# Kernel tuning notes

Measured on AMD Instinct MI355X. Metric: run time of the kernel, lower is better.

The kernel has to match this reference:

```python
import jax, jax.numpy as jnp
import numpy as np

D_MODEL = 1024
NUM_HEADS = 16
HEAD_DIM = D_MODEL // NUM_HEADS
THETA = 10000.0


def setup_inputs() -> dict:
    key = jax.random.key(0)
    k1, k2, k3 = jax.random.split(key, 3)
    B, S = 4, 2048
    x = jax.random.normal(k1, (B, S, D_MODEL), dtype=jnp.float32)
    token_positions = jnp.arange(S, dtype=jnp.int32)
    std_qkv = 2.0 / (D_MODEL + 3 * D_MODEL)
    std_o = 2.0 / (D_MODEL + D_MODEL)
    W_qkv = jax.random.normal(k2, (3 * D_MODEL, D_MODEL), dtype=jnp.float32) * std_qkv
    W_o = jax.random.normal(k3, (D_MODEL, D_MODEL), dtype=jnp.float32) * std_o
    return {"x": x, "token_positions": token_positions, "W_qkv": W_qkv, "W_o": W_o}


def _apply_rope(x, positions):
    # x: [B, H, S, d]; positions: [S]
    d = x.shape[-1]
    inv_freq = 1.0 / THETA ** (2.0 * jnp.arange(0, d // 2, dtype=jnp.float32) / d)
    angle = positions.astype(jnp.float32)[:, None] * inv_freq[None, :]  # [S, d/2]
    cos, sin = jnp.cos(angle), jnp.sin(angle)
    x1, x2 = x[..., 0::2], x[..., 1::2]
    rot = jnp.stack([x1 * cos - x2 * sin, x2 * cos + x1 * sin], axis=-1)
    return rot.reshape(x.shape)


def reference(x, token_positions, W_qkv, W_o):
    B, S, D = x.shape
    H, hd = NUM_HEADS, HEAD_DIM
    qkv = jnp.einsum('bsi,ji->bsj', x, W_qkv)            # [B, S, 3D]
    qkv = qkv.reshape(B, S, 3, H, hd).transpose(2, 0, 3, 1, 4)  # [3, B, H, S, hd]
    q, k, v = qkv[0], qkv[1], qkv[2]
    q = _apply_rope(q, token_positions)
    k = _apply_rope(k, token_positions)
    scores = jnp.einsum('bhqd,bhkd->bhqk', q, k) / jnp.sqrt(jnp.float32(hd))
    causal = jnp.tril(jnp.ones((S, S), dtype=bool))
    scores = jnp.where(causal, scores, -jnp.inf)
    probs = jax.nn.softmax(scores, axis=-1)
    attn = jnp.einsum('bhqk,bhkd->bhqd', probs, v)       # [B, H, S, hd]
    attn = attn.transpose(0, 2, 1, 3).reshape(B, S, D)
    return jnp.einsum('bsi,ji->bsj', attn, W_o)
```

## Files before the change

### kernel.cpp

```cpp
#include <hip/hip_runtime.h>

#define B_ 4
#define S_ 2048
#define D_ 1024
#define H_ 16
#define HD_ 64
#define M_ (B_*S_)
#define NQKV_ (3*D_)

typedef _Float16 f16;
typedef __attribute__((ext_vector_type(4))) _Float16 f16x4;
typedef __attribute__((ext_vector_type(8))) _Float16 f16x8;
typedef __attribute__((ext_vector_type(4))) float f32x4;

__device__ __forceinline__ void gload_lds16(const void* g, void* lds) {
  __builtin_amdgcn_global_load_lds(
      (const __attribute__((address_space(1))) void*)g,
      (__attribute__((address_space(3))) void*)lds, 16, 0, 0);
}

__global__ void cast_kernel(const float* __restrict__ in, f16* __restrict__ out) {
  size_t i = (size_t)(blockIdx.x * 256 + threadIdx.x) * 8;
  float4 a = *reinterpret_cast<const float4*>(in + i);
  float4 b = *reinterpret_cast<const float4*>(in + i + 4);
  f16x8 o;
  o[0] = (f16)a.x; o[1] = (f16)a.y; o[2] = (f16)a.z; o[3] = (f16)a.w;
  o[4] = (f16)b.x; o[5] = (f16)b.y; o[6] = (f16)b.z; o[7] = (f16)b.w;
  *reinterpret_cast<f16x8*>(out + i) = o;
}

__global__ void rope_kernel(f16* __restrict__ q, f16* __restrict__ k,
                            const int* __restrict__ pos) {
  int idx = blockIdx.x * 256 + threadIdx.x;
  int t = idx & 31;
  int srow = (idx >> 5) & (S_ - 1);
  float p = (float)pos[srow];
  float invf = exp2f((float)t * -0.4152410118609203f);
  float ang = p * invf;
  float sn, cs;
  sincosf(ang, &sn, &cs);
  const float qs = 0.125f * 1.4426950408889634f;
  size_t base = ((size_t)(idx >> 5)) * HD_ + 2 * t;
  float x1 = (float)q[base], x2 = (float)q[base + 1];
  q[base]     = (f16)((x1 * cs - x2 * sn) * qs);
  q[base + 1] = (f16)((x2 * cs + x1 * sn) * qs);
  x1 = (float)k[base]; x2 = (float)k[base + 1];
  k[base]     = (f16)(x1 * cs - x2 * sn);
  k[base + 1] = (f16)(x2 * cs + x1 * sn);
}

__global__ void vtrans_kernel(const f16* __restrict__ v, f16* __restrict__ vt) {
  __shared__ __align__(16) f16 tile[64][72];
  int tid = threadIdx.x;
  int bh = blockIdx.x >> 5;
  int s0 = (blockIdx.x & 31) << 6;
  const size_t vbase = ((size_t)bh * S_ + s0) * HD_;
  #pragma unroll
  for (int i = 0; i < 2; ++i) {
    int f = i * 256 + tid;
    int row = f >> 3, c8 = (f & 7) * 8;
    f16x8 val = *reinterpret_cast<const f16x8*>(v + vbase + (size_t)row * HD_ + c8);
    #pragma unroll
    for (int j = 0; j < 8; ++j) tile[row][c8 + j] = val[j];
  }
  __syncthreads();
  const size_t tbase = (size_t)bh * (HD_ * S_);
  #pragma unroll
  for (int i = 0; i < 2; ++i) {
    int f = i * 256 + tid;
    int d = f >> 3, c8 = (f & 7) * 8;
    f16x8 o;
    #pragma unroll
    for (int j = 0; j < 8; ++j) o[j] = tile[c8 + j][d];
    *reinterpret_cast<f16x8*>(vt + tbase + (size_t)d * S_ + s0 + c8) = o;
  }
}

template <int MODE>
__global__ __launch_bounds__(256)
void gemm_bt(const f16* __restrict__ A, const f16* __restrict__ Bt,
             void* __restrict__ Cout, int M, int N, int K) {
  __shared__ __align__(16) f16 As[128 * 64];
  __shared__ __align__(16) f16 Bs[128 * 64];
  const int tid = threadIdx.x;
  const int w = tid >> 6, l = tid & 63;
  const int nM = M >> 7;
  const int bm = (blockIdx.x % nM) << 7;
  const int bn = (blockIdx.x / nM) << 7;
  const int wr = (w >> 1) << 6;
  const int wc = (w & 1) << 6;
  const int lr = l & 15;
  const int lk = (l >> 4) << 3;
  const int orow = (l >> 4) << 2;
  const int srow = tid >> 3;
  const int sc8 = (tid & 7) * 8;

  f32x4 acc[4][4];
  #pragma unroll
  for (int i = 0; i < 4; ++i)
    #pragma unroll
    for (int j = 0; j < 4; ++j) acc[i][j] = f32x4{0.f, 0.f, 0.f, 0.f};

  for (int k0 = 0; k0 < K; k0 += 64) {
    __syncthreads();
    #pragma unroll
    for (int i = 0; i < 4; ++i) {
      gload_lds16(A + (size_t)(bm + i * 32 + srow) * K + k0 + sc8,
                  (void*)(As + (i * 256 + w * 64) * 8));
      gload_lds16(Bt + (size_t)(bn + i * 32 + srow) * K + k0 + sc8,
                  (void*)(Bs + (i * 256 + w * 64) * 8));
    }
    __syncthreads();
    #pragma unroll
    for (int t = 0; t < 2; ++t) {
      f16x8 af[4], bfr[4];
      #pragma unroll
      for (int mi = 0; mi < 4; ++mi)
        af[mi] = *reinterpret_cast<const f16x8*>(As + (wr + mi * 16 + lr) * 64 + t * 32 + lk);
      #pragma unroll
      for (int ni = 0; ni < 4; ++ni)
        bfr[ni] = *reinterpret_cast<const f16x8*>(Bs + (wc + ni * 16 + lr) * 64 + t * 32 + lk);
      #pragma unroll
      for (int mi = 0; mi < 4; ++mi)
        #pragma unroll
        for (int ni = 0; ni < 4; ++ni)
          acc[mi][ni] = __builtin_amdgcn_mfma_f32_16x16x32_f16(af[mi], bfr[ni], acc[mi][ni], 0, 0, 0);
    }
  }

  if (MODE == 0) {
    f16* qkv = (f16*)Cout;
    const size_t which_stride = (size_t)B_ * H_ * S_ * HD_;
    #pragma unroll
    for (int ni = 0; ni < 4; ++ni) {
      int n = bn + wc + ni * 16 + lr;
      int which = n >> 10, h = (n >> 6) & (H_ - 1), d = n & (HD_ - 1);
      size_t nb = (size_t)which * which_stride + (size_t)h * (S_ * HD_) + d;
      #pragma unroll
      for (int mi = 0; mi < 4; ++mi) {
        #pragma unroll
        for (int r = 0; r < 4; ++r) {
          int m = bm + wr + mi * 16 + orow + r;
          int b = m >> 11, s = m & (S_ - 1);
          qkv[nb + (size_t)b * (H_ * S_ * HD_) + (size_t)s * HD_] = (f16)acc[mi][ni][r];
        }
      }
    }
  } else {
    float* C = (float*)Cout;
    #pragma unroll
    for (int mi = 0; mi < 4; ++mi)
      #pragma unroll
      for (int r = 0; r < 4; ++r) {
        int m = bm + wr + mi * 16 + orow + r;
        #pragma unroll
        for (int ni = 0; ni < 4; ++ni) {
          int n = bn + wc + ni * 16 + lr;
          C[(size_t)m * N + n] = acc[mi][ni][r];
        }
      }
  }
}

__global__ __launch_bounds__(256)
void attn_kernel(const f16* __restrict__ q, const f16* __restrict__ k,
                 const f16* __restrict__ vt, f16* __restrict__ attn_out) {
  __shared__ __align__(16) f16 Ks[64 * 64];
  __shared__ __align__(16) f16 Vs[64 * 64];
  __shared__ __align__(16) f16 Ps[4][16 * 72];
  const int tid = threadIdx.x, w = tid >> 6, l = tid & 63;
  const int lr = l & 15, lk = (l >> 4) << 3, orow = (l >> 4) << 2;
  const int bh = blockIdx.x & 63;
  const int qt = 31 - (int)(blockIdx.x >> 6);
  const int q0 = qt << 6;
  const size_t bhoff = (size_t)bh * (S_ * HD_);
  const size_t vtoff = (size_t)bh * (HD_ * S_);
  const int srow = tid >> 3;
  const int sc8 = (tid & 7) * 8;
  const int ssw = sc8 ^ ((srow & 7) << 3);
  const int swz = (lr & 7) << 3;
  const int h = bh & (H_ - 1), b = bh >> 4;
  const int qg = q0 + w * 16 + lr;

  f16x8 qf[2];
  #pragma unroll
  for (int t = 0; t < 2; ++t)
    qf[t] = *reinterpret_cast<const f16x8*>(q + bhoff + (size_t)qg * HD_ + t * 32 + lk);

  f32x4 o[4];
  float m_run = -1e30f, l_run = 0.f;
  #pragma unroll
  for (int i = 0; i < 4; ++i) o[i] = f32x4{0.f, 0.f, 0.f, 0.f};

  const int ntiles = qt + 1;
  for (int it = 0; it < ntiles; ++it) {
    const int kv0 = it << 6;
    __syncthreads();
    #pragma unroll
    for (int i = 0; i < 2; ++i) {
      gload_lds16(k + bhoff + (size_t)(kv0 + i * 32 + srow) * HD_ + ssw,
                  (void*)(Ks + (i * 256 + w * 64) * 8));
      gload_lds16(vt + vtoff + (size_t)(i * 32 + srow) * S_ + kv0 + ssw,
                  (void*)(Vs + (i * 256 + w * 64) * 8));
    }
    __syncthreads();

    f32x4 sacc[4];
    #pragma unroll
    for (int ni = 0; ni < 4; ++ni) sacc[ni] = f32x4{0.f, 0.f, 0.f, 0.f};
    #pragma unroll
    for (int t = 0; t < 2; ++t) {
      #pragma unroll
      for (int ni = 0; ni < 4; ++ni) {
        f16x8 kf = *reinterpret_cast<const f16x8*>(Ks + (ni * 16 + lr) * 64 + ((t * 32 + lk) ^ swz));
        sacc[ni] = __builtin_amdgcn_mfma_f32_16x16x32_f16(kf, qf[t], sacc[ni], 0, 0, 0);
      }
    }
    if (it == ntiles - 1) {
      #pragma unroll
      for (int ni = 0; ni < 4; ++ni) {
        #pragma unroll
        for (int r = 0; r < 4; ++r) {
          int kvg = kv0 + ni * 16 + orow + r;
          if (kvg > qg) sacc[ni][r] = -1e30f;
        }
      }
    }

    f32x4 m4 = sacc[0];
    #pragma unroll
    for (int ni = 1; ni < 4; ++ni)
      #pragma unroll
      for (int r = 0; r < 4; ++r) m4[r] = fmaxf(m4[r], sacc[ni][r]);
    float mloc = fmaxf(fmaxf(m4[0], m4[1]), fmaxf(m4[2], m4[3]));
    mloc = fmaxf(mloc, __shfl_xor(mloc, 16));
    mloc = fmaxf(mloc, __shfl_xor(mloc, 32));
    float mn = fmaxf(m_run, mloc);
    float scale = exp2f(m_run - mn);
    m_run = mn;
    #pragma unroll
    for (int ni = 0; ni < 4; ++ni)
      #pragma unroll
      for (int r = 0; r < 4; ++r) sacc[ni][r] = exp2f(sacc[ni][r] - mn);
    f32x4 s4 = sacc[0];
    #pragma unroll
    for (int ni = 1; ni < 4; ++ni)
      #pragma unroll
      for (int r = 0; r < 4; ++r) s4[r] += sacc[ni][r];
    float sloc = (s4[0] + s4[1]) + (s4[2] + s4[3]);
    sloc += __shfl_xor(sloc, 16);
    sloc += __shfl_xor(sloc, 32);
    l_run = l_run * scale + sloc;
    #pragma unroll
    for (int ni = 0; ni < 4; ++ni)
      #pragma unroll
      for (int r = 0; r < 4; ++r) o[ni][r] *= scale;

    #pragma unroll
    for (int ni = 0; ni < 4; ++ni) {
      f16x4 pk;
      #pragma unroll
      for (int r = 0; r < 4; ++r) pk[r] = (f16)sacc[ni][r];
      *reinterpret_cast<f16x4*>(&Ps[w][lr * 72 + ni * 16 + orow]) = pk;
    }

    #pragma unroll
    for (int t = 0; t < 2; ++t) {
      f16x8 pf = *reinterpret_cast<const f16x8*>(&Ps[w][lr * 72 + t * 32 + lk]);
      #pragma unroll
      for (int ni = 0; ni < 4; ++ni) {
        f16x8 vf = *reinterpret_cast<const f16x8*>(Vs + (ni * 16 + lr) * 64 + ((t * 32 + lk) ^ swz));
        o[ni] = __builtin_amdgcn_mfma_f32_16x16x32_f16(vf, pf, o[ni], 0, 0, 0);
      }
    }
  }

  float rl = 1.0f / l_run;
  #pragma unroll
  for (int ni = 0; ni < 4; ++ni) {
    f16x4 ov;
    #pragma unroll
    for (int r = 0; r < 4; ++r) ov[r] = (f16)(o[ni][r] * rl);
    *reinterpret_cast<f16x4*>(
        &attn_out[(size_t)(b * S_ + qg) * D_ + h * HD_ + ni * 16 + orow]) = ov;
  }
}

extern "C" void kernel_launch(void* const* d_in, const int* in_sizes, int n_in,
                              void* d_out, int out_size, void* d_ws, size_t ws_size,
                              hipStream_t stream) {
  const float* x    = (const float*)d_in[0];
  const int*   pos  = (const int*)d_in[1];
  const float* wqkv = (const float*)d_in[2];
  const float* wo   = (const float*)d_in[3];
  float* out = (float*)d_out;

  const size_t BHSD = (size_t)B_ * H_ * S_ * HD_;
  f16* xb    = (f16*)d_ws;
  f16* wqkvb = xb + (size_t)M_ * D_;
  f16* wob   = wqkvb + (size_t)NQKV_ * D_;
  f16* qb    = wob + (size_t)D_ * D_;
  f16* kb    = qb + BHSD;
  f16* vb    = kb + BHSD;
  f16* vtb   = vb + BHSD;
  f16* attnb = vtb + BHSD;

  cast_kernel<<<(M_ * D_) / 2048, 256, 0, stream>>>(x, xb);
  cast_kernel<<<(NQKV_ * D_) / 2048, 256, 0, stream>>>(wqkv, wqkvb);
  cast_kernel<<<(D_ * D_) / 2048, 256, 0, stream>>>(wo, wob);

  gemm_bt<0><<<(M_ / 128) * (NQKV_ / 128), 256, 0, stream>>>(xb, wqkvb, (void*)qb, M_, NQKV_, D_);

  rope_kernel<<<(B_ * H_ * S_ * 32) / 256, 256, 0, stream>>>(qb, kb, pos);
  vtrans_kernel<<<B_ * H_ * (S_ / 64), 256, 0, stream>>>(vb, vtb);

  attn_kernel<<<64 * 32, 256, 0, stream>>>(qb, kb, vtb, attnb);

  gemm_bt<1><<<(M_ / 128) * (D_ / 128), 256, 0, stream>>>(attnb, wob, (void*)out, M_, D_, D_);
}
```

Measured before the change: 225.4 us.

## Fuse RoPE and V transpose into QKV GEMM epilogue via precomputed trig table

Swaps the MFMA operand order so each lane holds four consecutive output columns, which allows vectorized epilogue stores. The QKV GEMM epilogue now applies RoPE (with the softmax scale for Q) using a small precomputed cos/sin table and writes V directly in transposed layout. This removes the separate rope and vtrans kernels and their round trips through global memory. The output GEMM also gets float4 stores. The transposed V writes are strided scalar stores, which may be poorly coalesced.

Measured after the change: 216.2 us. 4.1% less time.

```diff
diff --git a/kernel.cpp b/kernel.cpp
--- a/kernel.cpp
+++ b/kernel.cpp
@@ -29,57 +29,22 @@
   *reinterpret_cast<f16x8*>(out + i) = o;
 }
 
-__global__ void rope_kernel(f16* __restrict__ q, f16* __restrict__ k,
-                            const int* __restrict__ pos) {
+__global__ void trig_kernel(const int* __restrict__ pos, float2* __restrict__ tab) {
   int idx = blockIdx.x * 256 + threadIdx.x;
-  int t = idx & 31;
-  int srow = (idx >> 5) & (S_ - 1);
-  float p = (float)pos[srow];
+  int s = idx >> 5, t = idx & 31;
+  float p = (float)pos[s];
   float invf = exp2f((float)t * -0.4152410118609203f);
-  float ang = p * invf;
   float sn, cs;
-  sincosf(ang, &sn, &cs);
-  const float qs = 0.125f * 1.4426950408889634f;
-  size_t base = ((size_t)(idx >> 5)) * HD_ + 2 * t;
-  float x1 = (float)q[base], x2 = (float)q[base + 1];
-  q[base]     = (f16)((x1 * cs - x2 * sn) * qs);
-  q[base + 1] = (f16)((x2 * cs + x1 * sn) * qs);
-  x1 = (float)k[base]; x2 = (float)k[base + 1];
-  k[base]     = (f16)(x1 * cs - x2 * sn);
-  k[base + 1] = (f16)(x2 * cs + x1 * sn);
-}
-
-__global__ void vtrans_kernel(const f16* __restrict__ v, f16* __restrict__ vt) {
-  __shared__ __align__(16) f16 tile[64][72];
-  int tid = threadIdx.x;
-  int bh = blockIdx.x >> 5;
-  int s0 = (blockIdx.x & 31) << 6;
-  const size_t vbase = ((size_t)bh * S_ + s0) * HD_;
-  #pragma unroll
-  for (int i = 0; i < 2; ++i) {
-    int f = i * 256 + tid;
-    int row = f >> 3, c8 = (f & 7) * 8;
-    f16x8 val = *reinterpret_cast<const f16x8*>(v + vbase + (size_t)row * HD_ + c8);
-    #pragma unroll
-    for (int j = 0; j < 8; ++j) tile[row][c8 + j] = val[j];
-  }
-  __syncthreads();
-  const size_t tbase = (size_t)bh * (HD_ * S_);
-  #pragma unroll
-  for (int i = 0; i < 2; ++i) {
-    int f = i * 256 + tid;
-    int d = f >> 3, c8 = (f & 7) * 8;
-    f16x8 o;
-    #pragma unroll
-    for (int j = 0; j < 8; ++j) o[j] = tile[c8 + j][d];
-    *reinterpret_cast<f16x8*>(vt + tbase + (size_t)d * S_ + s0 + c8) = o;
-  }
+  sincosf(p * invf, &sn, &cs);
+  tab[idx] = float2{cs, sn};
 }
 
 template <int MODE>
 __global__ __launch_bounds__(256)
 void gemm_bt(const f16* __restrict__ A, const f16* __restrict__ Bt,
-             void* __restrict__ Cout, int M, int N, int K) {
+             void* __restrict__ Cout, const float2* __restrict__ tab,
+             f16* __restrict__ kout, f16* __restrict__ vtout,
+             int M, int N, int K) {
   __shared__ __align__(16) f16 As[128 * 64];
   __shared__ __align__(16) f16 Bs[128 * 64];
   const int tid = threadIdx.x;
@@ -124,41 +89,61 @@
       for (int mi = 0; mi < 4; ++mi)
         #pragma unroll
         for (int ni = 0; ni < 4; ++ni)
-          acc[mi][ni] = __builtin_amdgcn_mfma_f32_16x16x32_f16(af[mi], bfr[ni], acc[mi][ni], 0, 0, 0);
+          acc[mi][ni] = __builtin_amdgcn_mfma_f32_16x16x32_f16(bfr[ni], af[mi], acc[mi][ni], 0, 0, 0);
     }
   }
 
   if (MODE == 0) {
-    f16* qkv = (f16*)Cout;
-    const size_t which_stride = (size_t)B_ * H_ * S_ * HD_;
-    #pragma unroll
-    for (int ni = 0; ni < 4; ++ni) {
-      int n = bn + wc + ni * 16 + lr;
-      int which = n >> 10, h = (n >> 6) & (H_ - 1), d = n & (HD_ - 1);
-      size_t nb = (size_t)which * which_stride + (size_t)h * (S_ * HD_) + d;
+    const int which = bn >> 10;
+    const int h = ((bn + wc) >> 6) & (H_ - 1);
+    if (which < 2) {
+      f16* dst = which ? kout : (f16*)Cout;
+      const float qs = which ? 1.0f : 0.125f * 1.4426950408889634f;
       #pragma unroll
       for (int mi = 0; mi < 4; ++mi) {
+        int m = bm + wr + mi * 16 + lr;
+        int b = m >> 11, s = m & (S_ - 1);
+        size_t rowbase = ((size_t)(b * H_ + h) * S_ + s) * HD_;
+        const float4* trow = reinterpret_cast<const float4*>(tab + (size_t)s * 32);
         #pragma unroll
-        for (int r = 0; r < 4; ++r) {
-          int m = bm + wr + mi * 16 + orow + r;
-          int b = m >> 11, s = m & (S_ - 1);
-          qkv[nb + (size_t)b * (H_ * S_ * HD_) + (size_t)s * HD_] = (f16)acc[mi][ni][r];
+        for (int ni = 0; ni < 4; ++ni) {
+          int d0 = ni * 16 + orow;
+          float4 cssn = trow[d0 >> 2];
+          float x0 = acc[mi][ni][0], x1 = acc[mi][ni][1];
+          float x2 = acc[mi][ni][2], x3 = acc[mi][ni][3];
+          f16x4 ov;
+          ov[0] = (f16)((x0 * cssn.x - x1 * cssn.y) * qs);
+          ov[1] = (f16)((x1 * cssn.x + x0 * cssn.y) * qs);
+          ov[2] = (f16)((x2 * cssn.z - x3 * cssn.w) * qs);
+          ov[3] = (f16)((x3 * cssn.z + x2 * cssn.w) * qs);
+          *reinterpret_cast<f16x4*>(&dst[rowbase + d0]) = ov;
         }
+      }
+    } else {
+      #pragma unroll
+      for (int mi = 0; mi < 4; ++mi) {
+        int m = bm + wr + mi * 16 + lr;
+        int b = m >> 11, s = m & (S_ - 1);
+        size_t base = (size_t)(b * H_ + h) * (HD_ * S_) + s;
+        #pragma unroll
+        for (int ni = 0; ni < 4; ++ni)
+          #pragma unroll
+          for (int r = 0; r < 4; ++r)
+            vtout[base + (size_t)(ni * 16 + orow + r) * S_] = (f16)acc[mi][ni][r];
       }
     }
   } else {
     float* C = (float*)Cout;
     #pragma unroll
-    for (int mi = 0; mi < 4; ++mi)
-      #pragma unroll
-      for (int r = 0; r < 4; ++r) {
-        int m = bm + wr + mi * 16 + orow + r;
-        #pragma unroll
-        for (int ni = 0; ni < 4; ++ni) {
-          int n = bn + wc + ni * 16 + lr;
-          C[(size_t)m * N + n] = acc[mi][ni][r];
-        }
-      }
+    for (int mi = 0; mi < 4; ++mi) {
+      int m = bm + wr + mi * 16 + lr;
+      #pragma unroll
+      for (int ni = 0; ni < 4; ++ni) {
+        int n = bn + wc + ni * 16 + orow;
+        *reinterpret_cast<float4*>(&C[(size_t)m * N + n]) =
+            float4{acc[mi][ni][0], acc[mi][ni][1], acc[mi][ni][2], acc[mi][ni][3]};
+      }
+    }
   }
 }
 
@@ -301,20 +286,20 @@
   f16* wob   = wqkvb + (size_t)NQKV_ * D_;
   f16* qb    = wob + (size_t)D_ * D_;
   f16* kb    = qb + BHSD;
-  f16* vb    = kb + BHSD;
-  f16* vtb   = vb + BHSD;
+  f16* vtb   = kb + BHSD;
   f16* attnb = vtb + BHSD;
+  float2* tab = (float2*)(attnb + BHSD);
 
   cast_kernel<<<(M_ * D_) / 2048, 256, 0, stream>>>(x, xb);
   cast_kernel<<<(NQKV_ * D_) / 2048, 256, 0, stream>>>(wqkv, wqkvb);
   cast_kernel<<<(D_ * D_) / 2048, 256, 0, stream>>>(wo, wob);
-
-  gemm_bt<0><<<(M_ / 128) * (NQKV_ / 128), 256, 0, stream>>>(xb, wqkvb, (void*)qb, M_, NQKV_, D_);
-
-  rope_kernel<<<(B_ * H_ * S_ * 32) / 256, 256, 0, stream>>>(qb, kb, pos);
-  vtrans_kernel<<<B_ * H_ * (S_ / 64), 256, 0, stream>>>(vb, vtb);
+  trig_kernel<<<(S_ * 32) / 256, 256, 0, stream>>>(pos, tab);
+
+  gemm_bt<0><<<(M_ / 128) * (NQKV_ / 128), 256, 0, stream>>>(
+      xb, wqkvb, (void*)qb, tab, kb, vtb, M_, NQKV_, D_);
 
   attn_kernel<<<64 * 32, 256, 0, stream>>>(qb, kb, vtb, attnb);
 
-  gemm_bt<1><<<(M_ / 128) * (D_ / 128), 256, 0, stream>>>(attnb, wob, (void*)out, M_, D_, D_);
-}
+  gemm_bt<1><<<(M_ / 128) * (D_ / 128), 256, 0, stream>>>(
+      attnb, wob, (void*)out, nullptr, nullptr, nullptr, M_, D_, D_);
+}
```
